# Performance work log

Measured on AMD Instinct MI355X. Metric: run time of the kernel, lower is better.

The kernel has to match this reference:

```python
import jax, jax.numpy as jnp
import numpy as np

B, T, V, LSRC, D = 4, 128, 50257, 512, 512
PAD_ID = 0
GAMMA1, GAMMA2 = 1.0, 0.1
BETA, MAX_ITER = 2.0, 400


def setup_inputs() -> dict:
    key = jax.random.key(0)
    ks = jax.random.split(key, 7)
    # output_mle are per-token probabilities (original takes torch.log of them)
    output_mle = jax.random.uniform(ks[0], (B, T, V), jnp.float32, 1e-4, 1.0)
    attn_dist = jax.random.uniform(ks[1], (B, LSRC, T), jnp.float32)
    coverage = jax.random.uniform(ks[2], (B, LSRC, T), jnp.float32)
    trg = jax.random.randint(ks[3], (B, T), 0, V)
    dec_mask = jax.random.randint(ks[4], (B, T), 0, 2).astype(bool)
    dec_len = jax.random.randint(ks[5], (B,), 1, T)
    W_emb = jax.random.normal(ks[6], (V, D), jnp.float32) * 0.02
    return {"output_mle": output_mle, "attn_dist": attn_dist, "coverage": coverage,
            "trg": trg, "dec_mask": dec_mask, "dec_len": dec_len, "W_emb": W_emb}


def ipot(a1, a2, beta=BETA, max_iter=MAX_ITER):
    # a1, a2: [n, d_hid] (already flattened from [B, T, d_hid])
    n = a1.shape[0]
    a1n = a1 / jnp.linalg.norm(a1, axis=1, keepdims=True)
    a2n = a2 / jnp.linalg.norm(a2, axis=1, keepdims=True)
    C = a1n @ a2n.T                      # [n, n] cosine cost
    A = jnp.exp(-C / beta)
    eye = jnp.eye(n, dtype=C.dtype)
    sigma0 = jnp.full((n, 1), 1.0 / n, C.dtype)
    T0 = jnp.full((n, n), 1.0 / (n * n), C.dtype)

    def step(carry, _):
        Tm, sigma = carry
        Q = A * Tm
        dvec = 1.0 / n / (Q @ sigma)          # [n, 1]
        sigma = 1.0 / n / (Q.T @ dvec)        # [n, 1]
        # Faithful to torch source: diag(d) * Q * diag(sigma) is ELEMENTWISE,
        # so only the diagonal of the product survives.
        Tm = dvec * Q * sigma.T * eye
        return (Tm, sigma), None

    (Tm, _), _ = jax.lax.scan(step, (T0, sigma0), None, length=max_iter)
    return jnp.sum(Tm * C)


def reference(output_mle, attn_dist, coverage, trg, dec_mask, dec_len, W_emb):
    # --- NLL loss (Eq. 6): mean -log p[target] over non-pad tokens ---
    logp = jnp.log(output_mle)
    tok_lp = jnp.take_along_axis(logp, trg[..., None], axis=-1)[..., 0]   # [B, T]
    valid = (trg != PAD_ID)
    nll = -jnp.sum(jnp.where(valid, tok_lp, 0.0)) / jnp.sum(valid).astype(logp.dtype)

    # --- Coverage loss (Eq. 12) ---
    cov = jnp.sum(jnp.minimum(attn_dist, coverage), axis=1)               # [B, T]
    cov = jnp.where(dec_mask, 0.0, cov)
    cov_loss = jnp.sum(cov) / jnp.sum(dec_len).astype(cov.dtype)

    # --- OT loss via IPOT ---
    trg_emb = W_emb[trg]                                                  # [B, T, D]
    probs = jax.nn.softmax(output_mle, axis=-1)
    pred = jnp.einsum('btv,vd->btd', probs, W_emb)                        # [B, T, D]
    ot = ipot(pred.reshape(-1, D), trg_emb.reshape(-1, D))

    # Faithful to source: gamma2 added as a constant (not multiplied by ot)
    return nll + GAMMA1 * cov_loss + GAMMA2 + ot
```

## Files before the change

### kernel.cpp

```cpp
#include <hip/hip_runtime.h>
#include <math.h>

#define B_ 4
#define T_ 128
#define V_ 50257
#define D_ 512
#define NROWS 512
#define GAMMA2_ 0.1f

#define BK 32
#define KC 1600
#define SPLITK 32
#define NIT (KC / BK)
#define LDA 40
#define LDB 40
#define SLICE (NROWS * D_)
#define WS_PART_OFF 1024

#define SPLITK2 48
#define KC2 1056
#define KP 50688
#define NXB 2048
#define XUPQ 792
#define NWB ((KP / 64) * (D_ / 64))
#define ACC_BYTES 4096
#define XB_BYTES ((size_t)NROWS * KP * 2)
#define WT_BYTES ((size_t)D_ * KP * 2)
#define PART2_BYTES ((size_t)SPLITK2 * SLICE * 4)
#define NEED_NEW (ACC_BYTES + XB_BYTES + WT_BYTES + PART2_BYTES)

typedef __attribute__((ext_vector_type(8))) short s8v;
typedef __attribute__((ext_vector_type(4))) float f4v;

__device__ inline unsigned int pack2bf(float f0, float f1) {
    unsigned int u0 = __float_as_uint(f0);
    unsigned int u1 = __float_as_uint(f1);
    u0 += 0x7fffu + ((u0 >> 16) & 1u);
    u1 += 0x7fffu + ((u1 >> 16) & 1u);
    return (u0 >> 16) | (u1 & 0xffff0000u);
}

__device__ inline void sync_lds() {
    __builtin_amdgcn_s_waitcnt(0xC07F);
    __builtin_amdgcn_s_barrier();
}

__device__ inline float wave_reduce(float v) {
    #pragma unroll
    for (int o = 32; o > 0; o >>= 1) v += __shfl_down(v, o, 64);
    return v;
}

__device__ __forceinline__ void gload16(const unsigned short* g, unsigned short* l) {
    __builtin_amdgcn_global_load_lds(
        (const __attribute__((address_space(1))) unsigned int*)g,
        (__attribute__((address_space(3))) unsigned int*)l, 16, 0, 0);
}

__device__ void misc_body(int bid,
                          const float* __restrict__ output_mle,
                          const float* __restrict__ attn,
                          const float* __restrict__ cover,
                          const int* __restrict__ trg,
                          const int* __restrict__ dec_mask,
                          const int* __restrict__ dec_len,
                          float* __restrict__ acc) {
    if (bid < 64) {
        float s = 0.f;
        const float4* a4 = (const float4*)attn;
        const float4* c4 = (const float4*)cover;
        for (int i4 = bid * 256 + threadIdx.x; i4 < 65536; i4 += 64 * 256) {
            float4 a = a4[i4];
            float4 c = c4[i4];
            int b = i4 >> 14;
            int t = (i4 << 2) & (T_ - 1);
            int4 m = *(const int4*)&dec_mask[(b << 7) + t];
            s += m.x ? 0.f : fminf(a.x, c.x);
            s += m.y ? 0.f : fminf(a.y, c.y);
            s += m.z ? 0.f : fminf(a.z, c.z);
            s += m.w ? 0.f : fminf(a.w, c.w);
        }
        s = wave_reduce(s);
        if ((threadIdx.x & 63) == 0) atomicAdd(&acc[2], s);
    } else {
        float lp = 0.f, cnt = 0.f;
        for (int i = threadIdx.x; i < NROWS; i += 256) {
            int tg = trg[i];
            if (tg != 0) {
                lp += __logf(output_mle[(size_t)i * V_ + tg]);
                cnt += 1.f;
            }
        }
        lp = wave_reduce(lp); cnt = wave_reduce(cnt);
        if ((threadIdx.x & 63) == 0) { atomicAdd(&acc[0], lp); atomicAdd(&acc[1], cnt); }
        if (threadIdx.x < B_) atomicAdd(&acc[3], (float)dec_len[threadIdx.x]);
    }
}

__global__ void misc_kernel(const float* __restrict__ output_mle,
                            const float* __restrict__ attn,
                            const float* __restrict__ cover,
                            const int* __restrict__ trg,
                            const int* __restrict__ dec_mask,
                            const int* __restrict__ dec_len,
                            float* __restrict__ acc) {
    misc_body(blockIdx.x, output_mle, attn, cover, trg, dec_mask, dec_len, acc);
}

__launch_bounds__(256)
__global__ void prep_kernel(const float* __restrict__ X,
                            const float* __restrict__ W,
                            const float* __restrict__ attn,
                            const float* __restrict__ cover,
                            const int* __restrict__ trg,
                            const int* __restrict__ dec_mask,
                            const int* __restrict__ dec_len,
                            float* __restrict__ acc,
                            unsigned short* __restrict__ Xb,
                            unsigned short* __restrict__ Wt) {
    const int bid = blockIdx.x;
    const int tid = threadIdx.x;
    if (bid < NXB) {
        const int row  = bid >> 2;
        const int q    = bid & 3;
        const int base = q * XUPQ;
        const float* src = X + (size_t)row * V_;
        unsigned short* dst = Xb + (size_t)row * KP;
        #pragma unroll 2
        for (int i = tid; i < XUPQ; i += 256) {
            int k16 = (base + i) << 4;
            unsigned int pk[8];
            if (k16 + 16 <= V_) {
                float4 v0 = *(const float4*)(src + k16);
                float4 v1 = *(const float4*)(src + k16 + 4);
                float4 v2 = *(const float4*)(src + k16 + 8);
                float4 v3 = *(const float4*)(src + k16 + 12);
                pk[0] = pack2bf(__expf(v0.x), __expf(v0.y));
                pk[1] = pack2bf(__expf(v0.z), __expf(v0.w));
                pk[2] = pack2bf(__expf(v1.x), __expf(v1.y));
                pk[3] = pack2bf(__expf(v1.z), __expf(v1.w));
                pk[4] = pack2bf(__expf(v2.x), __expf(v2.y));
                pk[5] = pack2bf(__expf(v2.z), __expf(v2.w));
                pk[6] = pack2bf(__expf(v3.x), __expf(v3.y));
                pk[7] = pack2bf(__expf(v3.z), __expf(v3.w));
            } else {
                #pragma unroll
                for (int p = 0; p < 8; p++) {
                    float e0 = (k16 + 2 * p     < V_) ? __expf(src[k16 + 2 * p])     : 0.f;
                    float e1 = (k16 + 2 * p + 1 < V_) ? __expf(src[k16 + 2 * p + 1]) : 0.f;
                    pk[p] = pack2bf(e0, e1);
                }
            }
            *(uint4*)&dst[k16]     = *(uint4*)&pk[0];
            *(uint4*)&dst[k16 + 8] = *(uint4*)&pk[4];
        }
    } else if (bid < NXB + NWB) {
        __shared__ float Ls[64][64];
        int w  = bid - NXB;
        int kt = w >> 3;
        int dt = w & 7;
        int k0 = kt << 6, d0 = dt << 6;
        int r0 = tid >> 4;
        int c0 = (tid & 15) << 2;
        #pragma unroll
        for (int q = 0; q < 4; q++) {
            int r  = (q << 4) + r0;
            int gk = k0 + r;
            float4 v;
            if (gk < V_) v = *(const float4*)&W[(size_t)gk * D_ + d0 + c0];
            else         v = make_float4(0.f, 0.f, 0.f, 0.f);
            int cr = (c0 + (r & 48)) & 63;
            *(float4*)&Ls[r][cr] = v;
        }
        __syncthreads();
        int d   = tid >> 2;
        int rb  = (tid & 3) << 4;
        int cr  = (d + rb) & 63;
        unsigned int pk[8];
        #pragma unroll
        for (int p = 0; p < 8; p++)
            pk[p] = pack2bf(Ls[rb + 2 * p][cr], Ls[rb + 2 * p + 1][cr]);
        unsigned short* dst = Wt + (size_t)(d0 + d) * KP + k0 + rb;
        *(uint4*)&dst[0] = *(uint4*)&pk[0];
        *(uint4*)&dst[8] = *(uint4*)&pk[4];
    } else {
        misc_body(bid - (NXB + NWB), X, attn, cover, trg, dec_mask, dec_len, acc);
    }
}

__launch_bounds__(256)
__global__ void gemm2_kernel(const unsigned short* __restrict__ Xb,
                             const unsigned short* __restrict__ Wt,
                             float* __restrict__ part) {
    __shared__ __align__(16) unsigned short As[2][128 * 32];
    __shared__ __align__(16) unsigned short Bs[2][128 * 32];

    const int bx   = blockIdx.x;
    const int tile = bx & 15;
    const int s    = bx >> 4;
    const int i0   = (tile & 3) * 128;
    const int d0   = (tile >> 2) * 128;
    const size_t ks = (size_t)s * KC2;

    const int tid  = threadIdx.x;
    const int lane = tid & 63;
    const int wave = tid >> 6;
    const int wm   = (wave & 1) * 64;
    const int wn   = (wave >> 1) * 64;
    const int l15  = lane & 15;
    const int l4   = lane >> 4;

    const int grow = wave * 16 + (lane >> 2);
    const int gk8  = (lane & 3) * 8;
    const unsigned short* gA0 = Xb + (size_t)(i0 + grow) * KP + ks + gk8;
    const unsigned short* gA1 = gA0 + (size_t)64 * KP;
    const unsigned short* gB0 = Wt + (size_t)(d0 + grow) * KP + ks + gk8;
    const unsigned short* gB1 = gB0 + (size_t)64 * KP;

    f4v acc[4][4];
    #pragma unroll
    for (int a = 0; a < 4; a++)
        #pragma unroll
        for (int b = 0; b < 4; b++) acc[a][b] = (f4v)0.f;

    auto stage = [&](unsigned short* Ab, unsigned short* Bb, int off) {
        gload16(gA0 + off, Ab + wave * 512);
        gload16(gA1 + off, Ab + wave * 512 + 2048);
        gload16(gB0 + off, Bb + wave * 512);
        gload16(gB1 + off, Bb + wave * 512 + 2048);
    };
    auto compute = [&](const unsigned short* Ab, const unsigned short* Bb) {
        s8v af[4], bfr[4];
        #pragma unroll
        for (int mi = 0; mi < 4; mi++)
            af[mi] = *(const s8v*)&Ab[(wm + mi * 16 + l15) * 32 + l4 * 8];
        #pragma unroll
        for (int ni = 0; ni < 4; ni++)
            bfr[ni] = *(const s8v*)&Bb[(wn + ni * 16 + l15) * 32 + l4 * 8];
        #pragma unroll
        for (int mi = 0; mi < 4; mi++)
            #pragma unroll
            for (int ni = 0; ni < 4; ni++)
                acc[mi][ni] = __builtin_amdgcn_mfma_f32_16x16x32_bf16(
                    af[mi], bfr[ni], acc[mi][ni], 0, 0, 0);
    };

    stage(As[0], Bs[0], 0);
    __syncthreads();
    #pragma unroll 1
    for (int it = 0; it + 2 < KC2 / 32; it += 2) {
        stage(As[1], Bs[1], (it + 1) * 32);
        compute(As[0], Bs[0]);
        __syncthreads();
        stage(As[0], Bs[0], (it + 2) * 32);
        compute(As[1], Bs[1]);
        __syncthreads();
    }
    compute(As[0], Bs[0]);

    float* dst = part + (size_t)s * SLICE;
    #pragma unroll
    for (int mi = 0; mi < 4; mi++) {
        #pragma unroll
        for (int ni = 0; ni < 4; ni++) {
            int col = d0 + wn + ni * 16 + l15;
            #pragma unroll
            for (int r = 0; r < 4; r++) {
                int row = i0 + wm + mi * 16 + l4 * 4 + r;
                dst[row * D_ + col] = acc[mi][ni][r];
            }
        }
    }
}

__launch_bounds__(256)
__global__ void gemm_kernel(const float* __restrict__ X,
                            const float* __restrict__ W,
                            float* __restrict__ part,
                            int use_atomic) {
    __shared__ __align__(16) short As[128 * LDA];
    __shared__ __align__(16) short Bs[128 * LDB];

    const int bx   = blockIdx.x;
    const int tile = bx & 15;
    const int s    = bx >> 4;
    const int i0   = (tile & 3) * 128;
    const int d0   = (tile >> 2) * 128;
    const int ks   = s * KC;
    const int ke   = min(ks + KC, V_);

    const int tid  = threadIdx.x;
    const int lane = tid & 63;
    const int wave = tid >> 6;
    const int wm   = (wave & 1) * 64;
    const int wn   = (wave >> 1) * 64;
    const int l15  = lane & 15;
    const int l4   = lane >> 4;

    const int ar   = tid >> 1;
    const int akh  = (tid & 1) * 16;
    const int bn2  = (tid & 63) * 2;
    const int bkq  = (tid >> 6) * 8;

    f4v acc[4][4];
    #pragma unroll
    for (int a = 0; a < 4; a++)
        #pragma unroll
        for (int b = 0; b < 4; b++) acc[a][b] = (f4v)0.f;

    auto stageA = [&](const float4 (&ab)[4]) {
        const float* f = (const float*)&ab[0];
        unsigned int au[8];
        #pragma unroll
        for (int p = 0; p < 8; p++)
            au[p] = pack2bf(__expf(f[2 * p]), __expf(f[2 * p + 1]));
        *(uint4*)&As[ar * LDA + akh]     = *(const uint4*)&au[0];
        *(uint4*)&As[ar * LDA + akh + 8] = *(const uint4*)&au[4];
    };
    auto stageB = [&](const float2 (&bb)[8]) {
        unsigned int r0[4], r1[4];
        #pragma unroll
        for (int p = 0; p < 4; p++) {
            r0[p] = pack2bf(bb[2 * p].x, bb[2 * p + 1].x);
            r1[p] = pack2bf(bb[2 * p].y, bb[2 * p + 1].y);
        }
        *(uint4*)&Bs[bn2 * LDB + bkq]       = *(const uint4*)&r0[0];
        *(uint4*)&Bs[(bn2 + 1) * LDB + bkq] = *(const uint4*)&r1[0];
    };
    auto domfma = [&]() {
        s8v af[4], bfr[4];
        #pragma unroll
        for (int mi = 0; mi < 4; mi++)
            af[mi] = *(const s8v*)&As[(wm + mi * 16 + l15) * LDA + l4 * 8];
        #pragma unroll
        for (int ni = 0; ni < 4; ni++)
            bfr[ni] = *(const s8v*)&Bs[(wn + ni * 16 + l15) * LDB + l4 * 8];
        #pragma unroll
        for (int mi = 0; mi < 4; mi++)
            #pragma unroll
            for (int ni = 0; ni < 4; ni++)
                acc[mi][ni] = __builtin_amdgcn_mfma_f32_16x16x32_bf16(
                    af[mi], bfr[ni], acc[mi][ni], 0, 0, 0);
    };
    auto issue = [&](float4 (&ab)[4], float2 (&bb)[8], const float* ap, const float* bp) {
        #pragma unroll
        for (int q = 0; q < 4; q++) ab[q] = *(const float4*)(ap + q * 4);
        #pragma unroll
        for (int j = 0; j < 8; j++) bb[j] = *(const float2*)(bp + (size_t)j * D_);
    };

    if (ks + KC <= V_) {
        const float* ap = X + (size_t)(i0 + ar) * V_ + ks + akh;
        const float* bp = W + d0 + bn2 + (size_t)(ks + bkq) * D_;
        float4 a0[4], a1[4];
        float2 b0[8], b1[8];
        issue(a0, b0, ap, bp);
        #pragma unroll 1
        for (int it = 0; it < NIT; it += 2) {
            ap += BK; bp += (size_t)BK * D_;
            if (it + 1 < NIT) issue(a1, b1, ap, bp);
            sync_lds();
            stageA(a0); stageB(b0);
            sync_lds();
            domfma();

            ap += BK; bp += (size_t)BK * D_;
            if (it + 2 < NIT) issue(a0, b0, ap, bp);
            sync_lds();
            stageA(a1); stageB(b1);
            sync_lds();
            domfma();
        }
    } else {
        const float* Abase = X + (size_t)(i0 + ar) * V_;
        const float* Bbase = W + d0 + bn2;
        for (int k0 = ks; k0 < ke; k0 += BK) {
            float4 ab[4];
            float2 bb[8];
            #pragma unroll
            for (int q = 0; q < 4; q++) {
                int gk = min(k0 + akh + q * 4, V_ - 4);
                ab[q] = *(const float4*)(Abase + gk);
            }
            #pragma unroll
            for (int j = 0; j < 8; j++) {
                int gk = min(k0 + bkq + j, V_ - 1);
                bb[j] = *(const float2*)(Bbase + (size_t)gk * D_);
            }
            sync_lds();
            {
                unsigned int au[8];
                const float* f = (const float*)&ab[0];
                #pragma unroll
                for (int p = 0; p < 8; p++) {
                    int g0 = k0 + akh + 2 * p;
                    float e0 = (g0     < ke) ? __expf(f[2 * p])     : 0.f;
                    float e1 = (g0 + 1 < ke) ? __expf(f[2 * p + 1]) : 0.f;
                    au[p] = pack2bf(e0, e1);
                }
                *(uint4*)&As[ar * LDA + akh]     = *(const uint4*)&au[0];
                *(uint4*)&As[ar * LDA + akh + 8] = *(const uint4*)&au[4];
            }
            {
                unsigned int r0[4], r1[4];
                #pragma unroll
                for (int p = 0; p < 4; p++) {
                    int g0 = k0 + bkq + 2 * p;
                    float x0 = (g0     < ke) ? bb[2 * p].x     : 0.f;
                    float x1 = (g0 + 1 < ke) ? bb[2 * p + 1].x : 0.f;
                    float y0 = (g0     < ke) ? bb[2 * p].y     : 0.f;
                    float y1 = (g0 + 1 < ke) ? bb[2 * p + 1].y : 0.f;
                    r0[p] = pack2bf(x0, x1);
                    r1[p] = pack2bf(y0, y1);
                }
                *(uint4*)&Bs[bn2 * LDB + bkq]       = *(const uint4*)&r0[0];
                *(uint4*)&Bs[(bn2 + 1) * LDB + bkq] = *(const uint4*)&r1[0];
            }
            sync_lds();
            domfma();
        }
    }

    float* dst = part + (use_atomic ? 0 : (size_t)s * SLICE);
    #pragma unroll
    for (int mi = 0; mi < 4; mi++) {
        #pragma unroll
        for (int ni = 0; ni < 4; ni++) {
            int col = d0 + wn + ni * 16 + l15;
            #pragma unroll
            for (int r = 0; r < 4; r++) {
                int row = i0 + wm + mi * 16 + l4 * 4 + r;
                if (use_atomic) atomicAdd(&dst[row * D_ + col], acc[mi][ni][r]);
                else            dst[row * D_ + col] = acc[mi][ni][r];
            }
        }
    }
}

__global__ void ot_kernel(const float* __restrict__ part,
                          const float* __restrict__ W,
                          const int* __restrict__ trg,
                          float* __restrict__ acc,
                          int nsl) {
    __shared__ float Ps[4][D_];
    int wave = threadIdx.x >> 6, lane = threadIdx.x & 63;
    int row  = blockIdx.x;
    const size_t off = (size_t)row * D_ + lane * 8;

    float4 p0 = {0, 0, 0, 0}, p1 = {0, 0, 0, 0};
    for (int s = wave; s < nsl; s += 4) {
        const float4* ps = (const float4*)(part + (size_t)s * SLICE + off);
        float4 q0 = ps[0], q1 = ps[1];
        p0.x += q0.x; p0.y += q0.y; p0.z += q0.z; p0.w += q0.w;
        p1.x += q1.x; p1.y += q1.y; p1.z += q1.z; p1.w += q1.w;
    }
    *(float4*)&Ps[wave][lane * 8]     = p0;
    *(float4*)&Ps[wave][lane * 8 + 4] = p1;
    __syncthreads();
    if (wave == 0) {
        float4 s0 = {0, 0, 0, 0}, s1 = {0, 0, 0, 0};
        #pragma unroll
        for (int w = 0; w < 4; w++) {
            float4 q0 = *(const float4*)&Ps[w][lane * 8];
            float4 q1 = *(const float4*)&Ps[w][lane * 8 + 4];
            s0.x += q0.x; s0.y += q0.y; s0.z += q0.z; s0.w += q0.w;
            s1.x += q1.x; s1.y += q1.y; s1.z += q1.z; s1.w += q1.w;
        }
        const float4* t4 = (const float4*)(W + (size_t)trg[row] * D_ + lane * 8);
        float4 t0 = t4[0], t1 = t4[1];

        float dot = s0.x * t0.x + s0.y * t0.y + s0.z * t0.z + s0.w * t0.w
                  + s1.x * t1.x + s1.y * t1.y + s1.z * t1.z + s1.w * t1.w;
        float nn  = s0.x * s0.x + s0.y * s0.y + s0.z * s0.z + s0.w * s0.w
                  + s1.x * s1.x + s1.y * s1.y + s1.z * s1.z + s1.w * s1.w;
        float tt  = t0.x * t0.x + t0.y * t0.y + t0.z * t0.z + t0.w * t0.w
                  + t1.x * t1.x + t1.y * t1.y + t1.z * t1.z + t1.w * t1.w;

        dot = wave_reduce(dot); nn = wave_reduce(nn); tt = wave_reduce(tt);
        if (lane == 0)
            atomicAdd(&acc[4], (dot / sqrtf(nn * tt)) * (1.0f / (float)NROWS));
    }
}

__global__ void finalize_kernel(const float* __restrict__ acc, float* __restrict__ out) {
    if (threadIdx.x == 0)
        out[0] = -acc[0] / acc[1] + acc[2] / acc[3] + GAMMA2_ + acc[4];
}

extern "C" void kernel_launch(void* const* d_in, const int* in_sizes, int n_in,
                              void* d_out, int out_size, void* d_ws, size_t ws_size,
                              hipStream_t stream) {
    const float* output_mle = (const float*)d_in[0];
    const float* attn       = (const float*)d_in[1];
    const float* cover      = (const float*)d_in[2];
    const int*   trg        = (const int*)d_in[3];
    const int*   dec_mask   = (const int*)d_in[4];
    const int*   dec_len    = (const int*)d_in[5];
    const float* W          = (const float*)d_in[6];
    float* out  = (float*)d_out;
    float* acc  = (float*)d_ws;

    const bool newpath = (ws_size >= NEED_NEW);

    if (newpath) {
        unsigned short* Xb = (unsigned short*)((char*)d_ws + ACC_BYTES);
        unsigned short* Wt = (unsigned short*)((char*)d_ws + ACC_BYTES + XB_BYTES);
        float* part2 = (float*)((char*)d_ws + ACC_BYTES + XB_BYTES + WT_BYTES);
        hipMemsetAsync(d_ws, 0, ACC_BYTES, stream);
        prep_kernel<<<NXB + NWB + 65, 256, 0, stream>>>(
            output_mle, W, attn, cover, trg, dec_mask, dec_len, acc, Xb, Wt);
        gemm2_kernel<<<16 * SPLITK2, 256, 0, stream>>>(Xb, Wt, part2);
        ot_kernel<<<NROWS, 256, 0, stream>>>(part2, W, trg, acc, SPLITK2);
        finalize_kernel<<<1, 64, 0, stream>>>(acc, out);
    } else {
        float* part = acc + WS_PART_OFF;
        const size_t need = (size_t)WS_PART_OFF * 4 + (size_t)SPLITK * SLICE * 4;
        const bool partial = (ws_size >= need);
        if (partial) {
            hipMemsetAsync(d_ws, 0, WS_PART_OFF * sizeof(float), stream);
        } else {
            hipMemsetAsync(d_ws, 0, (WS_PART_OFF + SLICE) * sizeof(float), stream);
        }
        misc_kernel<<<65, 256, 0, stream>>>(output_mle, attn, cover, trg, dec_mask, dec_len, acc);
        gemm_kernel<<<16 * SPLITK, 256, 0, stream>>>(output_mle, W, part, partial ? 0 : 1);
        ot_kernel<<<NROWS, 256, 0, stream>>>(part, W, trg, acc, partial ? SPLITK : 1);
        finalize_kernel<<<1, 64, 0, stream>>>(acc, out);
    }
}
```

Before: 340.3 us.

## Rework bf16 prep transposes and remap GEMM blocks for XCD-local K-slices

The W transpose to bf16 no longer stages 64x64 tiles through LDS. Each thread now reads 16 strided rows of one column directly: adjacent threads read adjacent d, so loads stay coalesced, and the thread writes 32 contiguous bytes of Wt. The X exp/convert grid is halved to two blocks per row with more unrolling. The GEMM block index is remapped so the 16 tiles of one K-slice land on the same XCD, with the aim of sharing their A/B reads in that XCD's L2. The trade-off is fewer, longer-running prep blocks and more global load instructions per thread.

Result: slower. 372.3 us (+9.4%).

```diff
diff --git a/kernel.cpp b/kernel.cpp
--- a/kernel.cpp
+++ b/kernel.cpp
@@ -20,9 +20,10 @@
 #define SPLITK2 48
 #define KC2 1056
 #define KP 50688
-#define NXB 2048
-#define XUPQ 792
-#define NWB ((KP / 64) * (D_ / 64))
+#define KU 3168
+#define NPB_X 1024
+#define NPB_W 1024
+#define WCELLS (D_ * KU)
 #define ACC_BYTES 4096
 #define XB_BYTES ((size_t)NROWS * KP * 2)
 #define WT_BYTES ((size_t)D_ * KP * 2)
@@ -120,14 +121,13 @@
                             unsigned short* __restrict__ Wt) {
     const int bid = blockIdx.x;
     const int tid = threadIdx.x;
-    if (bid < NXB) {
-        const int row  = bid >> 2;
-        const int q    = bid & 3;
-        const int base = q * XUPQ;
+    if (bid < NPB_X) {
+        const int row  = bid >> 1;
+        const int base = (bid & 1) * (KU / 2);
         const float* src = X + (size_t)row * V_;
         unsigned short* dst = Xb + (size_t)row * KP;
-        #pragma unroll 2
-        for (int i = tid; i < XUPQ; i += 256) {
+        #pragma unroll 4
+        for (int i = tid; i < KU / 2; i += 256) {
             int k16 = (base + i) << 4;
             unsigned int pk[8];
             if (k16 + 16 <= V_) {
@@ -154,37 +154,31 @@
             *(uint4*)&dst[k16]     = *(uint4*)&pk[0];
             *(uint4*)&dst[k16 + 8] = *(uint4*)&pk[4];
         }
-    } else if (bid < NXB + NWB) {
-        __shared__ float Ls[64][64];
-        int w  = bid - NXB;
-        int kt = w >> 3;
-        int dt = w & 7;
-        int k0 = kt << 6, d0 = dt << 6;
-        int r0 = tid >> 4;
-        int c0 = (tid & 15) << 2;
-        #pragma unroll
-        for (int q = 0; q < 4; q++) {
-            int r  = (q << 4) + r0;
-            int gk = k0 + r;
-            float4 v;
-            if (gk < V_) v = *(const float4*)&W[(size_t)gk * D_ + d0 + c0];
-            else         v = make_float4(0.f, 0.f, 0.f, 0.f);
-            int cr = (c0 + (r & 48)) & 63;
-            *(float4*)&Ls[r][cr] = v;
-        }
-        __syncthreads();
-        int d   = tid >> 2;
-        int rb  = (tid & 3) << 4;
-        int cr  = (d + rb) & 63;
-        unsigned int pk[8];
-        #pragma unroll
-        for (int p = 0; p < 8; p++)
-            pk[p] = pack2bf(Ls[rb + 2 * p][cr], Ls[rb + 2 * p + 1][cr]);
-        unsigned short* dst = Wt + (size_t)(d0 + d) * KP + k0 + rb;
-        *(uint4*)&dst[0] = *(uint4*)&pk[0];
-        *(uint4*)&dst[8] = *(uint4*)&pk[4];
+    } else if (bid < NPB_X + NPB_W) {
+        const int c0 = (bid - NPB_X) * 256 + tid;
+        #pragma unroll 2
+        for (int c = c0; c < WCELLS; c += NPB_W * 256) {
+            int d   = c & (D_ - 1);
+            int k16 = (c >> 9) << 4;
+            const float* src = W + d;
+            float v[16];
+            if (k16 + 16 <= V_) {
+                #pragma unroll
+                for (int j = 0; j < 16; j++) v[j] = src[(size_t)(k16 + j) * D_];
+            } else {
+                #pragma unroll
+                for (int j = 0; j < 16; j++)
+                    v[j] = (k16 + j < V_) ? src[(size_t)(k16 + j) * D_] : 0.f;
+            }
+            unsigned int pk[8];
+            #pragma unroll
+            for (int p = 0; p < 8; p++) pk[p] = pack2bf(v[2 * p], v[2 * p + 1]);
+            unsigned short* dst = Wt + (size_t)d * KP + k16;
+            *(uint4*)&dst[0] = *(uint4*)&pk[0];
+            *(uint4*)&dst[8] = *(uint4*)&pk[4];
+        }
     } else {
-        misc_body(bid - (NXB + NWB), X, attn, cover, trg, dec_mask, dec_len, acc);
+        misc_body(bid - (NPB_X + NPB_W), X, attn, cover, trg, dec_mask, dec_len, acc);
     }
 }
 
@@ -196,8 +190,10 @@
     __shared__ __align__(16) unsigned short Bs[2][128 * 32];
 
     const int bx   = blockIdx.x;
-    const int tile = bx & 15;
-    const int s    = bx >> 4;
+    const int xcd  = bx & 7;
+    const int j    = bx >> 3;
+    const int s    = xcd + 8 * (j >> 4);
+    const int tile = j & 15;
     const int i0   = (tile & 3) * 128;
     const int d0   = (tile >> 2) * 128;
     const size_t ks = (size_t)s * KC2;
@@ -507,7 +503,7 @@
         unsigned short* Wt = (unsigned short*)((char*)d_ws + ACC_BYTES + XB_BYTES);
         float* part2 = (float*)((char*)d_ws + ACC_BYTES + XB_BYTES + WT_BYTES);
         hipMemsetAsync(d_ws, 0, ACC_BYTES, stream);
-        prep_kernel<<<NXB + NWB + 65, 256, 0, stream>>>(
+        prep_kernel<<<NPB_X + NPB_W + 65, 256, 0, stream>>>(
             output_mle, W, attn, cover, trg, dec_mask, dec_len, acc, Xb, Wt);
         gemm2_kernel<<<16 * SPLITK2, 256, 0, stream>>>(Xb, Wt, part2);
         ot_kernel<<<NROWS, 256, 0, stream>>>(part2, W, trg, acc, SPLITK2);
```
